# Kernel optimization log

Hardware: AMD Instinct MI355X
Metric: run time of the kernel (lower is better)

The kernel has to match this reference:

```python
import jax, jax.numpy as jnp
import numpy as np


def setup_inputs() -> dict:
    key = jax.random.key(0)
    k1, k2 = jax.random.split(key)
    B, S, K, N = 2, 4096, 4096, 4096
    x = jax.random.randint(k1, (B, S, K), -127, 128, dtype=jnp.int32).astype(jnp.int8)
    weight = jax.random.randint(k2, (N, K), -127, 128, dtype=jnp.int32).astype(jnp.int8)
    bias = jnp.zeros((1, N), dtype=jnp.int8)
    a = jnp.float32(0.01)   # alpha = input_scale * weight_scale / output_scale
    b = jnp.float32(1.0)    # beta = bias_scale / output_scale
    return {"x": x, "weight": weight, "bias": bias, "a": a, "b": b}


def reference(x, weight, bias, a, b):
    # i8gemm.linear_a8_w8_b8_o8: int8 GEMM with int32 accumulation, then
    # y_int8 = saturate_cast(round(alpha * acc + beta * bias)).
    x_shape = x.shape
    xf = x.reshape(-1, x_shape[-1])                     # [M, K] int8
    acc = jnp.matmul(xf, weight.T, preferred_element_type=jnp.int32)  # [M, N]
    y = a * acc.astype(jnp.float32) + b * bias.astype(jnp.float32)    # fused epilogue
    yq = jnp.clip(jnp.round(y), -128.0, 127.0).astype(jnp.int8)       # requantize o8
    return yq.reshape(*x_shape[:-1], -1)
```

## Files before the change

### kernel.cpp

```cpp
#include <hip/hip_runtime.h>
#include <stdint.h>

#define M_DIM 8192
#define N_DIM 4096
#define K_DIM 4096

using int4v  = __attribute__((ext_vector_type(4))) int;
using int16v = __attribute__((ext_vector_type(16))) int;

__global__ __launch_bounds__(256) void pack_kernel(const int4* __restrict__ sx,
                                                   const int4* __restrict__ sw,
                                                   unsigned int* __restrict__ dst,
                                                   int nx, int ntot) {
    int idx = blockIdx.x * blockDim.x + threadIdx.x;
    if (idx >= ntot) return;
    int4 v = (idx < nx) ? sx[idx] : sw[idx - nx];
    dst[idx] = (v.x & 0xff) | ((v.y & 0xff) << 8) | ((v.z & 0xff) << 16) |
               ((v.w & 0xff) << 24);
}

__device__ __forceinline__ void async_copy16(const char* g, char* l) {
    __builtin_amdgcn_global_load_lds(
        (const __attribute__((address_space(1))) char*)g,
        (__attribute__((address_space(3))) char*)l, 16, 0, 0);
}

__global__ __launch_bounds__(256, 2) void gemm_i8_kernel(
    const char* __restrict__ Aq,
    const char* __restrict__ Bq,
    const int* __restrict__ bias,
    const float* __restrict__ a_ptr,
    const float* __restrict__ b_ptr,
    int32_t* __restrict__ out)
{
    __shared__ char As[128 * 64];
    __shared__ char Bs[128 * 64];

    const int tid  = threadIdx.x;
    const int lane = tid & 63;
    const int wave = tid >> 6;
    const int wr   = wave >> 1;
    const int wc   = wave & 1;
    const int m0   = blockIdx.y * 128;
    const int n0   = blockIdx.x * 128;

    const float alpha = *a_ptr;
    const float beta  = *b_ptr;

    int16v acc[2][2] = {};

    const int srow = tid >> 2;
    const int scol = (tid & 3) * 16;

    const char* aG0 = Aq + (size_t)(m0 + srow) * K_DIM + scol;
    const char* aG1 = aG0 + (size_t)64 * K_DIM;
    const char* bG0 = Bq + (size_t)(n0 + srow) * K_DIM + scol;
    const char* bG1 = bG0 + (size_t)64 * K_DIM;
    char* aL0 = &As[tid * 16];
    char* aL1 = &As[tid * 16 + 4096];
    char* bL0 = &Bs[tid * 16];
    char* bL1 = &Bs[tid * 16 + 4096];

    const int fm = lane & 31;
    const int fk = (lane >> 5) * 16;

    for (int k0 = 0; k0 < K_DIM; k0 += 64) {
        async_copy16(aG0 + k0, aL0);
        async_copy16(aG1 + k0, aL1);
        async_copy16(bG0 + k0, bL0);
        async_copy16(bG1 + k0, bL1);
        __syncthreads();

        int4v af[2][2], bf[2][2];
#pragma unroll
        for (int i = 0; i < 2; ++i)
#pragma unroll
            for (int kk = 0; kk < 2; ++kk) {
                af[i][kk] = *(const int4v*)
                    &As[(wr * 64 + i * 32 + fm) * 64 + kk * 32 + fk];
                bf[i][kk] = *(const int4v*)
                    &Bs[(wc * 64 + i * 32 + fm) * 64 + kk * 32 + fk];
            }

#pragma unroll
        for (int i = 0; i < 2; ++i)
#pragma unroll
            for (int j = 0; j < 2; ++j)
#pragma unroll
                for (int kk = 0; kk < 2; ++kk)
                    acc[i][j] = __builtin_amdgcn_mfma_i32_32x32x32_i8(
                        af[i][kk], bf[j][kk], acc[i][j], 0, 0, 0);

        __syncthreads();
    }

    const int ocol  = lane & 31;
    const int rbase = (lane >> 5) * 4;
#pragma unroll
    for (int j = 0; j < 2; ++j) {
        const int gn = n0 + wc * 64 + j * 32 + ocol;
        const float bb = beta * (float)bias[gn];
#pragma unroll
        for (int i = 0; i < 2; ++i) {
            const int gm = m0 + wr * 64 + i * 32;
#pragma unroll
            for (int r = 0; r < 16; ++r) {
                const int row = (r & 3) + 8 * (r >> 2) + rbase;
                float v = alpha * (float)acc[i][j][r] + bb;
                v = rintf(v);
                v = fminf(fmaxf(v, -128.0f), 127.0f);
                out[(size_t)(gm + row) * N_DIM + gn] = (int32_t)v;
            }
        }
    }
}

extern "C" void kernel_launch(void* const* d_in, const int* in_sizes, int n_in,
                              void* d_out, int out_size, void* d_ws, size_t ws_size,
                              hipStream_t stream) {
    const int*   x    = (const int*)d_in[0];
    const int*   w    = (const int*)d_in[1];
    const int*   bias = (const int*)d_in[2];
    const float* a    = (const float*)d_in[3];
    const float* b    = (const float*)d_in[4];
    int32_t*     out  = (int32_t*)d_out;

    char* xq = (char*)d_ws;
    const int nx   = (M_DIM * K_DIM) / 4;
    const int nw   = (N_DIM * K_DIM) / 4;
    const int ntot = nx + nw;
    pack_kernel<<<(ntot + 255) / 256, 256, 0, stream>>>(
        (const int4*)x, (const int4*)w, (unsigned int*)xq, nx, ntot);

    char* wq = xq + (size_t)M_DIM * K_DIM;

    dim3 grid(N_DIM / 128, M_DIM / 128);
    gemm_i8_kernel<<<grid, 256, 0, stream>>>(xq, wq, bias, a, b, out);
}
```

Baseline: 429.6 us.

## Enlarge GEMM tile to 256x256 with double-buffered LDS and XOR swizzle

Grows the block tile from 128x128 to 256x256, so each wave now computes 128x128 with a 4x4 set of MFMA accumulators. It adds double-buffered LDS, so the next K-slice loads asynchronously while the current one is computed. It also applies an XOR swizzle on LDS columns to reduce bank conflicts. These aim to raise arithmetic intensity and hide global load latency. In exchange, register pressure rises to 256 accumulator VGPRs with occupancy of one block per CU, and the grid shrinks to 512 blocks.

```diff
diff --git a/kernel.cpp b/kernel.cpp
--- a/kernel.cpp
+++ b/kernel.cpp
@@ -25,7 +25,7 @@
         (__attribute__((address_space(3))) char*)l, 16, 0, 0);
 }
 
-__global__ __launch_bounds__(256, 2) void gemm_i8_kernel(
+__global__ __launch_bounds__(256, 1) void gemm_i8_kernel(
     const char* __restrict__ Aq,
     const char* __restrict__ Bq,
     const int* __restrict__ bias,
@@ -33,63 +33,73 @@
     const float* __restrict__ b_ptr,
     int32_t* __restrict__ out)
 {
-    __shared__ char As[128 * 64];
-    __shared__ char Bs[128 * 64];
+    __shared__ char As[2][256 * 64];
+    __shared__ char Bs[2][256 * 64];
 
     const int tid  = threadIdx.x;
     const int lane = tid & 63;
     const int wave = tid >> 6;
     const int wr   = wave >> 1;
     const int wc   = wave & 1;
-    const int m0   = blockIdx.y * 128;
-    const int n0   = blockIdx.x * 128;
+    const int m0   = blockIdx.y * 256;
+    const int n0   = blockIdx.x * 256;
 
     const float alpha = *a_ptr;
     const float beta  = *b_ptr;
 
-    int16v acc[2][2] = {};
+    int16v acc[4][4] = {};
 
     const int srow = tid >> 2;
-    const int scol = (tid & 3) * 16;
+    const int scol = ((tid & 3) ^ ((srow >> 1) & 3)) * 16;
 
-    const char* aG0 = Aq + (size_t)(m0 + srow) * K_DIM + scol;
-    const char* aG1 = aG0 + (size_t)64 * K_DIM;
-    const char* bG0 = Bq + (size_t)(n0 + srow) * K_DIM + scol;
-    const char* bG1 = bG0 + (size_t)64 * K_DIM;
-    char* aL0 = &As[tid * 16];
-    char* aL1 = &As[tid * 16 + 4096];
-    char* bL0 = &Bs[tid * 16];
-    char* bL1 = &Bs[tid * 16 + 4096];
+    const char* aG = Aq + (size_t)(m0 + srow) * K_DIM + scol;
+    const char* bG = Bq + (size_t)(n0 + srow) * K_DIM + scol;
+    const size_t q64 = (size_t)64 * K_DIM;
+    const int l16 = tid * 16;
 
-    const int fm = lane & 31;
-    const int fk = (lane >> 5) * 16;
+    const int fr   = lane & 31;
+    const int gw   = lane >> 5;
+    const int fkey = (fr >> 1) & 3;
+
+#pragma unroll
+    for (int q = 0; q < 4; ++q) {
+        async_copy16(aG + q * q64, &As[0][l16 + 4096 * q]);
+        async_copy16(bG + q * q64, &Bs[0][l16 + 4096 * q]);
+    }
+    __syncthreads();
 
     for (int k0 = 0; k0 < K_DIM; k0 += 64) {
-        async_copy16(aG0 + k0, aL0);
-        async_copy16(aG1 + k0, aL1);
-        async_copy16(bG0 + k0, bL0);
-        async_copy16(bG1 + k0, bL1);
-        __syncthreads();
+        const int cur = (k0 >> 6) & 1;
+        const int nxt = cur ^ 1;
 
-        int4v af[2][2], bf[2][2];
+        if (k0 + 64 < K_DIM) {
 #pragma unroll
-        for (int i = 0; i < 2; ++i)
+            for (int q = 0; q < 4; ++q) {
+                async_copy16(aG + q * q64 + k0 + 64, &As[nxt][l16 + 4096 * q]);
+                async_copy16(bG + q * q64 + k0 + 64, &Bs[nxt][l16 + 4096 * q]);
+            }
+        }
+
+        int4v af[2][4], bf[2][4];
 #pragma unroll
-            for (int kk = 0; kk < 2; ++kk) {
-                af[i][kk] = *(const int4v*)
-                    &As[(wr * 64 + i * 32 + fm) * 64 + kk * 32 + fk];
-                bf[i][kk] = *(const int4v*)
-                    &Bs[(wc * 64 + i * 32 + fm) * 64 + kk * 32 + fk];
+        for (int kk = 0; kk < 2; ++kk)
+#pragma unroll
+            for (int i = 0; i < 4; ++i) {
+                const int co = (((2 * kk + gw) ^ fkey) * 16);
+                af[kk][i] = *(const int4v*)
+                    &As[cur][(wr * 128 + i * 32 + fr) * 64 + co];
+                bf[kk][i] = *(const int4v*)
+                    &Bs[cur][(wc * 128 + i * 32 + fr) * 64 + co];
             }
 
 #pragma unroll
-        for (int i = 0; i < 2; ++i)
+        for (int kk = 0; kk < 2; ++kk)
 #pragma unroll
-            for (int j = 0; j < 2; ++j)
+            for (int i = 0; i < 4; ++i)
 #pragma unroll
-                for (int kk = 0; kk < 2; ++kk)
+                for (int j = 0; j < 4; ++j)
                     acc[i][j] = __builtin_amdgcn_mfma_i32_32x32x32_i8(
-                        af[i][kk], bf[j][kk], acc[i][j], 0, 0, 0);
+                        af[kk][i], bf[kk][j], acc[i][j], 0, 0, 0);
 
         __syncthreads();
     }
@@ -97,12 +107,12 @@
     const int ocol  = lane & 31;
     const int rbase = (lane >> 5) * 4;
 #pragma unroll
-    for (int j = 0; j < 2; ++j) {
-        const int gn = n0 + wc * 64 + j * 32 + ocol;
+    for (int j = 0; j < 4; ++j) {
+        const int gn = n0 + wc * 128 + j * 32 + ocol;
         const float bb = beta * (float)bias[gn];
 #pragma unroll
-        for (int i = 0; i < 2; ++i) {
-            const int gm = m0 + wr * 64 + i * 32;
+        for (int i = 0; i < 4; ++i) {
+            const int gm = m0 + wr * 128 + i * 32;
 #pragma unroll
             for (int r = 0; r < 16; ++r) {
                 const int row = (r & 3) + 8 * (r >> 2) + rbase;
@@ -134,6 +144,6 @@
 
     char* wq = xq + (size_t)M_DIM * K_DIM;
 
-    dim3 grid(N_DIM / 128, M_DIM / 128);
+    dim3 grid(N_DIM / 256, M_DIM / 256);
     gemm_i8_kernel<<<grid, 256, 0, stream>>>(xq, wq, bias, a, b, out);
 }
```

New measurement: 472.1 us. 9.9% more time.
